# Performance work log

Measured on AMD Instinct MI355X. Metric: run time of the kernel, lower is better.

## Reference

```python
import jax, jax.numpy as jnp
import numpy as np

NUM_ITERS = 20  # fixed in the original forward: transcribe(dna, iterations=20)


def transcribe(dna_seed, dna_a, dna_b):
    """Fractal DNA decompression: 20 elementwise contractive-map iterations
    over the full weight tensor, starting from the DNA seed."""
    def step(w, ab):
        a, b = ab
        w = a * w + b * jnp.sin(w)
        return w, None
    w, _ = jax.lax.scan(step, dna_seed, (dna_a, dna_b))
    return w  # [out_features, in_features]


def setup_inputs() -> dict:
    key = jax.random.key(0)
    k1, k2, k3, k4, k5 = jax.random.split(key, 5)
    TOKENS, IN_F, OUT_F = 2048, 4096, 4096
    return {
        "x": jax.random.normal(k1, (TOKENS, IN_F), dtype=jnp.float32),
        "dna_seed": jax.random.normal(k2, (OUT_F, IN_F), dtype=jnp.float32),
        "dna_a": jax.random.uniform(k3, (NUM_ITERS,), dtype=jnp.float32),
        "dna_b": jax.random.uniform(k4, (NUM_ITERS,), dtype=jnp.float32),
        "bias": jax.random.normal(k5, (OUT_F,), dtype=jnp.float32),
    }


def reference(x, dna_seed, dna_a, dna_b, bias):
    weight = transcribe(dna_seed, dna_a, dna_b)          # [out, in]
    # F.linear(x, weight, bias) == x @ weight.T + bias
    return jnp.einsum('ti,oi->to', x, weight) + bias     # [tokens, out]
```

## Files before the change

kernel.cpp:

```cpp
#include <hip/hip_runtime.h>
#include <hip/hip_bf16.h>

typedef __attribute__((ext_vector_type(8))) short short8;
typedef __attribute__((ext_vector_type(4))) float floatx4;

#define TOKENS 2048
#define IN_F   4096
#define OUT_F  4096
#define NITER  20

#define INV_2PI 0.15915494309189535f

__device__ __forceinline__ unsigned short f2bf(float f) {
    unsigned int u = __builtin_bit_cast(unsigned int, f);
    u += 0x7fffu + ((u >> 16) & 1u);
    return (unsigned short)(u >> 16);
}

__device__ __forceinline__ float hw_sin(float x) {
    return __builtin_amdgcn_sinf(x * INV_2PI);
}

template <int ITERS>
__global__ __launch_bounds__(256) void transcribe_kernel(
    const float4* __restrict__ in,
    const float* __restrict__ da, const float* __restrict__ db,
    ushort* __restrict__ out, int nvec)
{
    int i = blockIdx.x * 256 + threadIdx.x;
    if (i >= nvec) return;
    float4 w = in[i];
#pragma unroll
    for (int t = 0; t < ITERS; t++) {
        float a = da[t], b = db[t];
        w.x = a * w.x + b * hw_sin(w.x);
        w.y = a * w.y + b * hw_sin(w.y);
        w.z = a * w.z + b * hw_sin(w.z);
        w.w = a * w.w + b * hw_sin(w.w);
    }
    ushort4 o;
    o.x = f2bf(w.x); o.y = f2bf(w.y); o.z = f2bf(w.z); o.w = f2bf(w.w);
    *(ushort4*)(out + 4 * (size_t)i) = o;
}

__device__ __forceinline__ void g2l16(const ushort* g, ushort* l) {
    __builtin_amdgcn_global_load_lds(
        (const __attribute__((address_space(1))) unsigned int*)g,
        (__attribute__((address_space(3))) unsigned int*)l, 16, 0, 0);
}

__global__ __launch_bounds__(256) void gemm_bt_kernel(
    const ushort* __restrict__ A,
    const ushort* __restrict__ B,
    const float* __restrict__ bias,
    float* __restrict__ C,
    int M, int N, int K)
{
    __shared__ ushort As[128 * 32];
    __shared__ ushort Bs[128 * 32];

    const int tid  = threadIdx.x;
    const int lane = tid & 63;
    const int wid  = tid >> 6;
    const int bn   = blockIdx.x;
    const int bm   = blockIdx.y;
    const int wm   = (wid >> 1) << 6;
    const int wn   = (wid & 1) << 6;
    const int fm   = lane & 15;
    const int fkd  = (((lane >> 4) ^ ((fm >> 1) & 3)) << 3);

    const int row0 = tid >> 2;
    const int psg  = tid & 3;
    const int gsg  = (psg ^ ((row0 >> 1) & 3)) << 3;
    const int lsg  = psg << 3;

    const ushort* gA = A + (size_t)(bm * 128) * K;
    const ushort* gB = B + (size_t)(bn * 128) * K;

    floatx4 acc[4][4];
#pragma unroll
    for (int i = 0; i < 4; i++)
#pragma unroll
        for (int j = 0; j < 4; j++)
            acc[i][j] = (floatx4){0.f, 0.f, 0.f, 0.f};

    for (int k0 = 0; k0 < K; k0 += 32) {
        g2l16(gA + (size_t)row0 * K + k0 + gsg,        As + row0 * 32 + lsg);
        g2l16(gA + (size_t)(row0 + 64) * K + k0 + gsg, As + (row0 + 64) * 32 + lsg);
        g2l16(gB + (size_t)row0 * K + k0 + gsg,        Bs + row0 * 32 + lsg);
        g2l16(gB + (size_t)(row0 + 64) * K + k0 + gsg, Bs + (row0 + 64) * 32 + lsg);
        __syncthreads();

        short8 af[4], bfr[4];
#pragma unroll
        for (int i = 0; i < 4; i++)
            af[i] = *(const short8*)(As + (wm + i * 16 + fm) * 32 + fkd);
#pragma unroll
        for (int j = 0; j < 4; j++)
            bfr[j] = *(const short8*)(Bs + (wn + j * 16 + fm) * 32 + fkd);
#pragma unroll
        for (int i = 0; i < 4; i++)
#pragma unroll
            for (int j = 0; j < 4; j++)
                acc[i][j] = __builtin_amdgcn_mfma_f32_16x16x32_bf16(
                    af[i], bfr[j], acc[i][j], 0, 0, 0);
        __syncthreads();
    }

    const int cn = lane & 15;
    const int cm = (lane >> 4) << 2;
    float bv[4];
#pragma unroll
    for (int j = 0; j < 4; j++)
        bv[j] = bias[bn * 128 + wn + j * 16 + cn];
#pragma unroll
    for (int i = 0; i < 4; i++) {
#pragma unroll
        for (int r = 0; r < 4; r++) {
            int m = bm * 128 + wm + i * 16 + cm + r;
            float* crow = C + (size_t)m * N + bn * 128 + wn + cn;
#pragma unroll
            for (int j = 0; j < 4; j++)
                crow[j * 16] = acc[i][j][r] + bv[j];
        }
    }
}

extern "C" void kernel_launch(void* const* d_in, const int* in_sizes, int n_in,
                              void* d_out, int out_size, void* d_ws, size_t ws_size,
                              hipStream_t stream) {
    const float* x    = (const float*)d_in[0];
    const float* seed = (const float*)d_in[1];
    const float* da   = (const float*)d_in[2];
    const float* db   = (const float*)d_in[3];
    const float* bias = (const float*)d_in[4];
    float* out        = (float*)d_out;

    ushort* w_bf = (ushort*)d_ws;
    ushort* x_bf = w_bf + (size_t)OUT_F * IN_F;

    const int nvec_w = OUT_F * IN_F / 4;
    const int nvec_x = TOKENS * IN_F / 4;

    transcribe_kernel<NITER><<<nvec_w / 256, 256, 0, stream>>>(
        (const float4*)seed, da, db, w_bf, nvec_w);
    transcribe_kernel<0><<<nvec_x / 256, 256, 0, stream>>>(
        (const float4*)x, da, db, x_bf, nvec_x);

    dim3 grid(OUT_F / 128, TOKENS / 128);
    gemm_bt_kernel<<<grid, 256, 0, stream>>>(x_bf, w_bf, bias, out,
                                             TOKENS, OUT_F, IN_F);
}
```

Measured before the change: 249.3 us.

## Halve GEMM M-tile to 64 and scale transcribe iterations into sin-unit domain

The GEMM block tile goes from 128x128 to 64x128, which doubles the grid to 1024 blocks and halves per-wave accumulators, to improve occupancy and CU load balance. The transcribe kernel keeps the weight in units of 2π across iterations, so the per-element multiply by 1/2π before each hardware sin is folded into a single pre- and post-scale plus a prescaled b coefficient. Each thread now handles 8 elements and writes one 16-byte store. The smaller M tile lowers arithmetic intensity and raises global/LDS traffic per FLOP, and the rescaled recurrence can round slightly differently.

Result: faster. 242.3 us (-2.8%).

```diff
diff --git a/kernel.cpp b/kernel.cpp
--- a/kernel.cpp
+++ b/kernel.cpp
@@ -10,6 +10,7 @@
 #define NITER  20
 
 #define INV_2PI 0.15915494309189535f
+#define TWO_PI  6.283185307179586f
 
 __device__ __forceinline__ unsigned short f2bf(float f) {
     unsigned int u = __builtin_bit_cast(unsigned int, f);
@@ -17,30 +18,41 @@
     return (unsigned short)(u >> 16);
 }
 
-__device__ __forceinline__ float hw_sin(float x) {
-    return __builtin_amdgcn_sinf(x * INV_2PI);
+__device__ __forceinline__ void step4(float4& v, float a, float bc) {
+    v.x = __builtin_fmaf(bc, __builtin_amdgcn_sinf(v.x), a * v.x);
+    v.y = __builtin_fmaf(bc, __builtin_amdgcn_sinf(v.y), a * v.y);
+    v.z = __builtin_fmaf(bc, __builtin_amdgcn_sinf(v.z), a * v.z);
+    v.w = __builtin_fmaf(bc, __builtin_amdgcn_sinf(v.w), a * v.w);
 }
 
 template <int ITERS>
 __global__ __launch_bounds__(256) void transcribe_kernel(
     const float4* __restrict__ in,
     const float* __restrict__ da, const float* __restrict__ db,
-    ushort* __restrict__ out, int nvec)
+    short8* __restrict__ out, int n8)
 {
     int i = blockIdx.x * 256 + threadIdx.x;
-    if (i >= nvec) return;
-    float4 w = in[i];
+    if (i >= n8) return;
+    float4 u = in[2 * i];
+    float4 v = in[2 * i + 1];
+    float fin = 1.0f;
+    if (ITERS > 0) {
+        u.x *= INV_2PI; u.y *= INV_2PI; u.z *= INV_2PI; u.w *= INV_2PI;
+        v.x *= INV_2PI; v.y *= INV_2PI; v.z *= INV_2PI; v.w *= INV_2PI;
 #pragma unroll
-    for (int t = 0; t < ITERS; t++) {
-        float a = da[t], b = db[t];
-        w.x = a * w.x + b * hw_sin(w.x);
-        w.y = a * w.y + b * hw_sin(w.y);
-        w.z = a * w.z + b * hw_sin(w.z);
-        w.w = a * w.w + b * hw_sin(w.w);
+        for (int t = 0; t < ITERS; t++) {
+            float a = da[t], bc = db[t] * INV_2PI;
+            step4(u, a, bc);
+            step4(v, a, bc);
+        }
+        fin = TWO_PI;
     }
-    ushort4 o;
-    o.x = f2bf(w.x); o.y = f2bf(w.y); o.z = f2bf(w.z); o.w = f2bf(w.w);
-    *(ushort4*)(out + 4 * (size_t)i) = o;
+    short8 o;
+    o[0] = (short)f2bf(u.x * fin); o[1] = (short)f2bf(u.y * fin);
+    o[2] = (short)f2bf(u.z * fin); o[3] = (short)f2bf(u.w * fin);
+    o[4] = (short)f2bf(v.x * fin); o[5] = (short)f2bf(v.y * fin);
+    o[6] = (short)f2bf(v.z * fin); o[7] = (short)f2bf(v.w * fin);
+    out[i] = o;
 }
 
 __device__ __forceinline__ void g2l16(const ushort* g, ushort* l) {
@@ -56,7 +68,7 @@
     float* __restrict__ C,
     int M, int N, int K)
 {
-    __shared__ ushort As[128 * 32];
+    __shared__ ushort As[64 * 32];
     __shared__ ushort Bs[128 * 32];
 
     const int tid  = threadIdx.x;
@@ -64,7 +76,7 @@
     const int wid  = tid >> 6;
     const int bn   = blockIdx.x;
     const int bm   = blockIdx.y;
-    const int wm   = (wid >> 1) << 6;
+    const int wm   = (wid >> 1) << 5;
     const int wn   = (wid & 1) << 6;
     const int fm   = lane & 15;
     const int fkd  = (((lane >> 4) ^ ((fm >> 1) & 3)) << 3);
@@ -74,32 +86,31 @@
     const int gsg  = (psg ^ ((row0 >> 1) & 3)) << 3;
     const int lsg  = psg << 3;
 
-    const ushort* gA = A + (size_t)(bm * 128) * K;
+    const ushort* gA = A + (size_t)(bm * 64) * K;
     const ushort* gB = B + (size_t)(bn * 128) * K;
 
-    floatx4 acc[4][4];
+    floatx4 acc[2][4];
 #pragma unroll
-    for (int i = 0; i < 4; i++)
+    for (int i = 0; i < 2; i++)
 #pragma unroll
         for (int j = 0; j < 4; j++)
             acc[i][j] = (floatx4){0.f, 0.f, 0.f, 0.f};
 
     for (int k0 = 0; k0 < K; k0 += 32) {
         g2l16(gA + (size_t)row0 * K + k0 + gsg,        As + row0 * 32 + lsg);
-        g2l16(gA + (size_t)(row0 + 64) * K + k0 + gsg, As + (row0 + 64) * 32 + lsg);
         g2l16(gB + (size_t)row0 * K + k0 + gsg,        Bs + row0 * 32 + lsg);
         g2l16(gB + (size_t)(row0 + 64) * K + k0 + gsg, Bs + (row0 + 64) * 32 + lsg);
         __syncthreads();
 
-        short8 af[4], bfr[4];
+        short8 af[2], bfr[4];
 #pragma unroll
-        for (int i = 0; i < 4; i++)
+        for (int i = 0; i < 2; i++)
             af[i] = *(const short8*)(As + (wm + i * 16 + fm) * 32 + fkd);
 #pragma unroll
         for (int j = 0; j < 4; j++)
             bfr[j] = *(const short8*)(Bs + (wn + j * 16 + fm) * 32 + fkd);
 #pragma unroll
-        for (int i = 0; i < 4; i++)
+        for (int i = 0; i < 2; i++)
 #pragma unroll
             for (int j = 0; j < 4; j++)
                 acc[i][j] = __builtin_amdgcn_mfma_f32_16x16x32_bf16(
@@ -114,10 +125,10 @@
     for (int j = 0; j < 4; j++)
         bv[j] = bias[bn * 128 + wn + j * 16 + cn];
 #pragma unroll
-    for (int i = 0; i < 4; i++) {
+    for (int i = 0; i < 2; i++) {
 #pragma unroll
         for (int r = 0; r < 4; r++) {
-            int m = bm * 128 + wm + i * 16 + cm + r;
+            int m = bm * 64 + wm + i * 16 + cm + r;
             float* crow = C + (size_t)m * N + bn * 128 + wn + cn;
 #pragma unroll
             for (int j = 0; j < 4; j++)
@@ -139,15 +150,15 @@
     ushort* w_bf = (ushort*)d_ws;
     ushort* x_bf = w_bf + (size_t)OUT_F * IN_F;
 
-    const int nvec_w = OUT_F * IN_F / 4;
-    const int nvec_x = TOKENS * IN_F / 4;
+    const int n8_w = OUT_F * IN_F / 8;
+    const int n8_x = TOKENS * IN_F / 8;
 
-    transcribe_kernel<NITER><<<nvec_w / 256, 256, 0, stream>>>(
-        (const float4*)seed, da, db, w_bf, nvec_w);
-    transcribe_kernel<0><<<nvec_x / 256, 256, 0, stream>>>(
-        (const float4*)x, da, db, x_bf, nvec_x);
+    transcribe_kernel<NITER><<<n8_w / 256, 256, 0, stream>>>(
+        (const float4*)seed, da, db, (short8*)w_bf, n8_w);
+    transcribe_kernel<0><<<n8_x / 256, 256, 0, stream>>>(
+        (const float4*)x, da, db, (short8*)x_bf, n8_x);
 
-    dim3 grid(OUT_F / 128, TOKENS / 128);
+    dim3 grid(OUT_F / 128, TOKENS / 64);
     gemm_bt_kernel<<<grid, 256, 0, stream>>>(x_bf, w_bf, bias, out,
                                              TOKENS, OUT_F, IN_F);
 }
```
